# Kernel tuning notes

Hardware: AMD Instinct MI355X
Metric: run time of the kernel (lower is better)

## Reference

```python
import jax, jax.numpy as jnp
import numpy as np

N_M, N_E = 100_000, 50_000      # materials / elements node counts
FM, FE, H = 256, 64, 128        # raw feature dims, hidden_channels
E, EL = 1_000_000, 250_000      # message edges per direction, label edges per decoder


def setup_inputs() -> dict:
    key = jax.random.key(0)
    ks = jax.random.split(key, 40)

    def w(i, shape):
        fan_in = shape[0]
        return jax.random.normal(ks[i], shape, jnp.float32) / np.sqrt(fan_in)

    inp = {
        "x_materials": jax.random.normal(ks[0], (N_M, FM), jnp.float32),
        "x_elements": jax.random.normal(ks[1], (N_E, FE), jnp.float32),
        # message-passing edges: materials->elements and elements->materials
        "src_m2e": jax.random.randint(ks[2], (E,), 0, N_M),
        "dst_m2e": jax.random.randint(ks[3], (E,), 0, N_E),
        "src_e2m": jax.random.randint(ks[4], (E,), 0, N_E),
        "dst_e2m": jax.random.randint(ks[5], (E,), 0, N_M),
        # supervision (edge_label_index) per decoder
        "lbl_src_m2e": jax.random.randint(ks[6], (EL,), 0, N_M),
        "lbl_dst_m2e": jax.random.randint(ks[7], (EL,), 0, N_E),
        "lbl_src_e2m": jax.random.randint(ks[8], (EL,), 0, N_E),
        "lbl_dst_e2m": jax.random.randint(ks[9], (EL,), 0, N_M),
        # input projections per node type
        "Wp_m": w(10, (FM, H)), "bp_m": jnp.zeros((H,), jnp.float32),
        "Wp_e": w(11, (FE, H)), "bp_e": jnp.zeros((H,), jnp.float32),
        # SAGEConv per edge type: lin_l (neighbor, with bias) + lin_r (root, no bias)
        "Wl_m2e": w(12, (H, H)), "bl_m2e": jnp.zeros((H,), jnp.float32), "Wr_m2e": w(13, (H, H)),
        "Wl_e2m": w(14, (H, H)), "bl_e2m": jnp.zeros((H,), jnp.float32), "Wr_e2m": w(15, (H, H)),
        # ffw linear per node type (to_hetero duplicates per node type)
        "Wffw_m": w(16, (H, H)), "bffw_m": jnp.zeros((H,), jnp.float32),
        "Wffw_e": w(17, (H, H)), "bffw_e": jnp.zeros((H,), jnp.float32),
        # output proj per node type
        "Wproj_m": w(18, (H, H)), "bproj_m": jnp.zeros((H,), jnp.float32),
        "Wproj_e": w(19, (H, H)), "bproj_e": jnp.zeros((H,), jnp.float32),
        # edge decoders (concat -> 2H -> 2H relu -> 1 -> sigmoid), one per edge type
        "Wmlp_m2e": w(20, (2 * H, 2 * H)), "bmlp_m2e": jnp.zeros((2 * H,), jnp.float32),
        "Wout_m2e": w(21, (2 * H, 1)), "bout_m2e": jnp.zeros((1,), jnp.float32),
        "Wmlp_e2m": w(22, (2 * H, 2 * H)), "bmlp_e2m": jnp.zeros((2 * H,), jnp.float32),
        "Wout_e2m": w(23, (2 * H, 1)), "bout_e2m": jnp.zeros((1,), jnp.float32),
    }
    return inp


def _sage(x_src, x_dst, src, dst, Wl, bl, Wr):
    """SAGEConv(aggr='mean'): W_l @ mean_{j in N(i)} x_j + b_l + W_r @ x_i."""
    n_dst = x_dst.shape[0]
    agg = jax.ops.segment_sum(x_src[src], dst, num_segments=n_dst)          # [n_dst, H]
    cnt = jax.ops.segment_sum(jnp.ones(src.shape, x_src.dtype), dst, num_segments=n_dst)
    mean = agg / jnp.maximum(cnt, 1.0)[:, None]
    return mean @ Wl + bl + x_dst @ Wr


def _decode(zs, zd, W1, b1, W2, b2):
    z = jnp.concatenate([zs, zd], axis=-1)                                  # [EL, 2H]
    z = jax.nn.relu(z @ W1 + b1)
    return jax.nn.sigmoid((z @ W2 + b2)[:, 0])                              # [EL]


def reference(x_materials, x_elements,
              src_m2e, dst_m2e, src_e2m, dst_e2m,
              lbl_src_m2e, lbl_dst_m2e, lbl_src_e2m, lbl_dst_e2m,
              Wp_m, bp_m, Wp_e, bp_e,
              Wl_m2e, bl_m2e, Wr_m2e, Wl_e2m, bl_e2m, Wr_e2m,
              Wffw_m, bffw_m, Wffw_e, bffw_e,
              Wproj_m, bproj_m, Wproj_e, bproj_e,
              Wmlp_m2e, bmlp_m2e, Wout_m2e, bout_m2e,
              Wmlp_e2m, bmlp_e2m, Wout_e2m, bout_e2m):
    # process_input_nodes: per-type projections
    z_m = x_materials @ Wp_m + bp_m
    z_e = x_elements @ Wp_e + bp_e
    # hetero SAGEConv layer (each node type has exactly one incoming edge type)
    h_m = jax.nn.relu(_sage(z_e, z_m, src_e2m, dst_e2m, Wl_e2m, bl_e2m, Wr_e2m))
    h_e = jax.nn.relu(_sage(z_m, z_e, src_m2e, dst_m2e, Wl_m2e, bl_m2e, Wr_m2e))
    # ffw layer per node type
    h_m = jax.nn.relu(h_m @ Wffw_m + bffw_m)
    h_e = jax.nn.relu(h_e @ Wffw_e + bffw_e)
    # output projection per node type
    h_m = h_m @ Wproj_m + bproj_m
    h_e = h_e @ Wproj_e + bproj_e
    # per-edge-type decoders on supervision edges
    out_m2e = _decode(h_m[lbl_src_m2e], h_e[lbl_dst_m2e], Wmlp_m2e, bmlp_m2e, Wout_m2e, bout_m2e)
    out_e2m = _decode(h_e[lbl_src_e2m], h_m[lbl_dst_e2m], Wmlp_e2m, bmlp_e2m, Wout_e2m, bout_e2m)
    return out_m2e, out_e2m
```

## Files before the change

kernel.cpp:

```cpp
#include <hip/hip_runtime.h>
#include <math.h>

#define N_M 100000
#define N_E 50000
#define FM 256
#define FE 64
#define H 128
#define NEDGE 1000000
#define NLBL 250000

#define BUCK 128
#define NB_M ((N_M + BUCK - 1) / BUCK)
#define NB_E ((N_E + BUCK - 1) / BUCK)
#define CAP_M 2048
#define CAP_E 4096
#define CHUNK 8192

typedef unsigned short u16;
typedef unsigned int u32;
typedef short bf16x8 __attribute__((ext_vector_type(8)));
typedef float f32x4  __attribute__((ext_vector_type(4)));
typedef u16 u16x8    __attribute__((ext_vector_type(8)));
typedef u16 u16x4    __attribute__((ext_vector_type(4)));

__device__ __forceinline__ u16 f2bf(float x) {
    unsigned u = __float_as_uint(x);
    u += 0x7FFF + ((u >> 16) & 1);
    return (u16)(u >> 16);
}
__device__ __forceinline__ float bf2f(u16 h) {
    return __uint_as_float(((unsigned)h) << 16);
}

#define NPACK 14
struct PackDesc { const float* src; u16* dst; int K, N; };
struct PackArgs { PackDesc d[NPACK]; };

__global__ __launch_bounds__(64)
void pack_kernel(PackArgs args)
{
    PackDesc pd = args.d[blockIdx.y];
    int KT = pd.K / 32, NT = pd.N / 16;
    int tile = blockIdx.x;
    if (tile >= KT * NT) return;
    int kt = tile / NT, nt = tile % NT;
    int l = threadIdx.x;
    u16* dst = pd.dst + ((size_t)tile * 64 + l) * 8;
    #pragma unroll
    for (int j = 0; j < 8; ++j) {
        float v = pd.src[(size_t)(kt * 32 + (l >> 4) * 8 + j) * pd.N + nt * 16 + (l & 15)];
        dst[j] = f2bf(v);
    }
}

template<int K, int N, bool HAS_A2, bool RELU, bool A_FP32, bool HAS_BIAS>
__global__ __launch_bounds__(256)
void mfma_gemm(const void* __restrict__ A1, const void* __restrict__ A2,
               const u16* __restrict__ W1p, const u16* __restrict__ W2p,
               const float* __restrict__ bias, u16* __restrict__ C, int M)
{
    constexpr int NT = N / 16, KT = K / 32;
    const int wid = threadIdx.x >> 6, lane = threadIdx.x & 63;
    const int row0 = blockIdx.x * 64 + wid * 16;
    if (row0 >= M) return;
    const int l15 = lane & 15, l4 = lane >> 4;

    f32x4 acc[NT];
    #pragma unroll
    for (int nt = 0; nt < NT; ++nt) acc[nt] = (f32x4){0.f, 0.f, 0.f, 0.f};

    const int npass = HAS_A2 ? 2 : 1;
    for (int pass = 0; pass < npass; ++pass) {
        const void* A = pass ? A2 : A1;
        const u16* Wp = pass ? W2p : W1p;
        #pragma unroll
        for (int kt = 0; kt < KT; ++kt) {
            bf16x8 a;
            if constexpr (A_FP32) {
                const float* ap = (const float*)A + (size_t)(row0 + l15) * K + kt * 32 + l4 * 8;
                float4 f0 = *(const float4*)ap;
                float4 f1 = *(const float4*)(ap + 4);
                a[0] = (short)f2bf(f0.x); a[1] = (short)f2bf(f0.y);
                a[2] = (short)f2bf(f0.z); a[3] = (short)f2bf(f0.w);
                a[4] = (short)f2bf(f1.x); a[5] = (short)f2bf(f1.y);
                a[6] = (short)f2bf(f1.z); a[7] = (short)f2bf(f1.w);
            } else {
                a = *(const bf16x8*)((const u16*)A + (size_t)(row0 + l15) * K + kt * 32 + l4 * 8);
            }
            #pragma unroll
            for (int nt = 0; nt < NT; ++nt) {
                bf16x8 b = *(const bf16x8*)(Wp + ((size_t)(kt * NT + nt) * 64 + lane) * 8);
                acc[nt] = __builtin_amdgcn_mfma_f32_16x16x32_bf16(a, b, acc[nt], 0, 0, 0);
            }
        }
    }

    #pragma unroll
    for (int nt = 0; nt < NT; ++nt) {
        #pragma unroll
        for (int r = 0; r < 4; ++r) {
            int row = row0 + l4 * 4 + r;
            int col = nt * 16 + l15;
            float v = acc[nt][r];
            if (HAS_BIAS) v += bias[col];
            if (RELU) v = fmaxf(v, 0.f);
            C[(size_t)row * N + col] = f2bf(v);
        }
    }
}

__global__ __launch_bounds__(1024)
void bucket2_kernel(const int* __restrict__ src_a, const int* __restrict__ dst_a,
                    const int* __restrict__ src_b, const int* __restrict__ dst_b,
                    u32* __restrict__ pairs_a, int* __restrict__ gcur_a,
                    u32* __restrict__ pairs_b, int* __restrict__ gcur_b)
{
    __shared__ int cnt[1024];
    __shared__ int gbase[1024];

    const int dir = blockIdx.y;
    const int* __restrict__ src = dir ? src_b : src_a;
    const int* __restrict__ dst = dir ? dst_b : dst_a;
    u32* __restrict__ pairs = dir ? pairs_b : pairs_a;
    int* __restrict__ gcur  = dir ? gcur_b : gcur_a;
    const int NB  = dir ? NB_E : NB_M;
    const int CAP = dir ? CAP_E : CAP_M;

    const int tid = threadIdx.x;
    const int e0 = blockIdx.x * CHUNK;
    const int e1 = min(e0 + CHUNK, NEDGE);

    cnt[tid] = 0;
    __syncthreads();

    int myd[CHUNK / 1024];
    int k = 0;
    for (int e = e0 + tid; e < e1; e += 1024, ++k) {
        int d = dst[e];
        myd[k] = d;
        atomicAdd(&cnt[d >> 7], 1);
    }
    __syncthreads();

    if (tid < NB) {
        int c = cnt[tid];
        gbase[tid] = (c > 0) ? atomicAdd(&gcur[tid], c) : 0;
        cnt[tid] = 0;
    }
    __syncthreads();

    k = 0;
    for (int e = e0 + tid; e < e1; e += 1024, ++k) {
        int d = myd[k];
        int b = d >> 7;
        int p = gbase[b] + atomicAdd(&cnt[b], 1);
        if (p < CAP)
            pairs[(size_t)b * CAP + p] = ((u32)(d & (BUCK - 1)) << 24) | (u32)src[e];
    }
}

__global__ __launch_bounds__(256)
void bucket_mean2_kernel(const u16* __restrict__ z_a, const u32* __restrict__ pairs_a,
                         const int* __restrict__ gcur_a, u16* __restrict__ out_a,
                         const u16* __restrict__ z_b, const u32* __restrict__ pairs_b,
                         const int* __restrict__ gcur_b, u16* __restrict__ out_b)
{
    __shared__ int loc_src[CAP_E];
    __shared__ int cnt[BUCK], seg[BUCK], cur[BUCK];

    const int dir = blockIdx.y;
    const int b = blockIdx.x;
    if (dir && b >= NB_E) return;

    const u16* __restrict__ z     = dir ? z_b : z_a;
    const u32* __restrict__ pairs = dir ? pairs_b : pairs_a;
    const int* __restrict__ gcur  = dir ? gcur_b : gcur_a;
    u16* __restrict__ outm        = dir ? out_b : out_a;
    const int cap     = dir ? CAP_E : CAP_M;
    const int n_nodes = dir ? N_E : N_M;

    const int tid = threadIdx.x;
    const int n = min(gcur[b], cap);
    const u32* __restrict__ pb = pairs + (size_t)b * cap;

    if (tid < BUCK) cnt[tid] = 0;
    __syncthreads();
    for (int e = tid; e < n; e += 256)
        atomicAdd(&cnt[pb[e] >> 24], 1);
    __syncthreads();

    int myc = (tid < BUCK) ? cnt[tid] : 0;
    if (tid < BUCK) seg[tid] = myc;
    __syncthreads();
    for (int off = 1; off < BUCK; off <<= 1) {
        int t = 0;
        if (tid < BUCK && tid >= off) t = seg[tid - off];
        __syncthreads();
        if (tid < BUCK && tid >= off) seg[tid] += t;
        __syncthreads();
    }
    if (tid < BUCK) { int ex = seg[tid] - myc; seg[tid] = ex; cur[tid] = ex; }
    __syncthreads();

    for (int e = tid; e < n; e += 256) {
        u32 pk = pb[e];
        int p = atomicAdd(&cur[pk >> 24], 1);
        loc_src[p] = (int)(pk & 0xFFFFFF);
    }
    __syncthreads();

    const int grp = tid >> 5, lane = tid & 31;
    for (int loc = grp; loc < BUCK; loc += 8) {
        int gnode = b * BUCK + loc;
        if (gnode >= n_nodes) continue;
        int s0 = seg[loc], c = cnt[loc];
        float4 accA = {0.f, 0.f, 0.f, 0.f};
        float4 accB = {0.f, 0.f, 0.f, 0.f};
        int i = 0;
        for (; i + 2 <= c; i += 2) {
            int sA = loc_src[s0 + i];
            int sB = loc_src[s0 + i + 1];
            u16x4 vA = *(const u16x4*)&z[(size_t)sA * H + lane * 4];
            u16x4 vB = *(const u16x4*)&z[(size_t)sB * H + lane * 4];
            accA.x += bf2f(vA[0]); accA.y += bf2f(vA[1]);
            accA.z += bf2f(vA[2]); accA.w += bf2f(vA[3]);
            accB.x += bf2f(vB[0]); accB.y += bf2f(vB[1]);
            accB.z += bf2f(vB[2]); accB.w += bf2f(vB[3]);
        }
        if (i < c) {
            int sA = loc_src[s0 + i];
            u16x4 vA = *(const u16x4*)&z[(size_t)sA * H + lane * 4];
            accA.x += bf2f(vA[0]); accA.y += bf2f(vA[1]);
            accA.z += bf2f(vA[2]); accA.w += bf2f(vA[3]);
        }
        accA.x += accB.x; accA.y += accB.y; accA.z += accB.z; accA.w += accB.w;
        float inv = 1.0f / fmaxf((float)c, 1.0f);
        u16x4 o;
        o[0] = f2bf(accA.x * inv); o[1] = f2bf(accA.y * inv);
        o[2] = f2bf(accA.z * inv); o[3] = f2bf(accA.w * inv);
        *(u16x4*)&outm[(size_t)gnode * H + lane * 4] = o;
    }
}

#define EPQ 8
#define NQ  31250

__global__ __launch_bounds__(256)
void edge_decode_kernel(const u16* __restrict__ Us, const u16* __restrict__ Ud,
                        const int* __restrict__ lsrc, const int* __restrict__ ldst,
                        const float* __restrict__ b1, const float* __restrict__ W2,
                        const float* __restrict__ b2, float* __restrict__ out)
{
    const int t  = blockIdx.x * 256 + threadIdx.x;
    const int q  = t >> 4;
    const int li = t & 15;
    if (q >= NQ) return;

    float w2v[16], b1v[16];
    #pragma unroll
    for (int j = 0; j < 4; ++j) {
        float4 w = *(const float4*)&W2[li * 16 + j * 4];
        float4 bb = *(const float4*)&b1[li * 16 + j * 4];
        w2v[j*4+0] = w.x; w2v[j*4+1] = w.y; w2v[j*4+2] = w.z; w2v[j*4+3] = w.w;
        b1v[j*4+0] = bb.x; b1v[j*4+1] = bb.y; b1v[j*4+2] = bb.z; b1v[j*4+3] = bb.w;
    }
    const float bout = b2[0];

    #pragma unroll
    for (int i = 0; i < EPQ; ++i) {
        int e = q + i * NQ;
        int s = lsrc[e], d = ldst[e];
        const u16* us = Us + (size_t)s * 256 + li * 16;
        const u16* ud = Ud + (size_t)d * 256 + li * 16;
        u16x8 sa = *(const u16x8*)us;
        u16x8 sb = *(const u16x8*)(us + 8);
        u16x8 da = *(const u16x8*)ud;
        u16x8 db = *(const u16x8*)(ud + 8);
        float acc = 0.f;
        #pragma unroll
        for (int j = 0; j < 8; ++j)
            acc += fmaxf(bf2f(sa[j]) + bf2f(da[j]) + b1v[j], 0.f) * w2v[j];
        #pragma unroll
        for (int j = 0; j < 8; ++j)
            acc += fmaxf(bf2f(sb[j]) + bf2f(db[j]) + b1v[8 + j], 0.f) * w2v[8 + j];
        acc += __shfl_xor(acc, 1, 16);
        acc += __shfl_xor(acc, 2, 16);
        acc += __shfl_xor(acc, 4, 16);
        acc += __shfl_xor(acc, 8, 16);
        if (li == 0) out[e] = 1.0f / (1.0f + expf(-(acc + bout)));
    }
}

extern "C" void kernel_launch(void* const* d_in, const int* in_sizes, int n_in,
                              void* d_out, int out_size, void* d_ws, size_t ws_size,
                              hipStream_t stream)
{
    const float* x_m      = (const float*)d_in[0];
    const float* x_e      = (const float*)d_in[1];
    const int*   src_m2e  = (const int*)d_in[2];
    const int*   dst_m2e  = (const int*)d_in[3];
    const int*   src_e2m  = (const int*)d_in[4];
    const int*   dst_e2m  = (const int*)d_in[5];
    const int*   lsrc_m2e = (const int*)d_in[6];
    const int*   ldst_m2e = (const int*)d_in[7];
    const int*   lsrc_e2m = (const int*)d_in[8];
    const int*   ldst_e2m = (const int*)d_in[9];
    const float* Wp_m   = (const float*)d_in[10];
    const float* bp_m   = (const float*)d_in[11];
    const float* Wp_e   = (const float*)d_in[12];
    const float* bp_e   = (const float*)d_in[13];
    const float* Wl_m2e = (const float*)d_in[14];
    const float* bl_m2e = (const float*)d_in[15];
    const float* Wr_m2e = (const float*)d_in[16];
    const float* Wl_e2m = (const float*)d_in[17];
    const float* bl_e2m = (const float*)d_in[18];
    const float* Wr_e2m = (const float*)d_in[19];
    const float* Wffw_m = (const float*)d_in[20];
    const float* bffw_m = (const float*)d_in[21];
    const float* Wffw_e = (const float*)d_in[22];
    const float* bffw_e = (const float*)d_in[23];
    const float* Wproj_m = (const float*)d_in[24];
    const float* bproj_m = (const float*)d_in[25];
    const float* Wproj_e = (const float*)d_in[26];
    const float* bproj_e = (const float*)d_in[27];
    const float* Wmlp_m2e = (const float*)d_in[28];
    const float* bmlp_m2e = (const float*)d_in[29];
    const float* Wout_m2e = (const float*)d_in[30];
    const float* bout_m2e = (const float*)d_in[31];
    const float* Wmlp_e2m = (const float*)d_in[32];
    const float* bmlp_e2m = (const float*)d_in[33];
    const float* Wout_e2m = (const float*)d_in[34];
    const float* bout_e2m = (const float*)d_in[35];

    float* out = (float*)d_out;

    u16* B_m = (u16*)d_ws;
    u16* B_e = B_m + (size_t)N_M * H;
    u16* U0  = B_e + (size_t)N_E * H;
    u16* A_m = U0;
    u16* A_e = A_m + (size_t)N_M * H;
    u16* Us  = U0;
    u16* Ud  = U0 + (size_t)N_M * 256;
    u32* pairs_m = (u32*)(A_e + (size_t)N_E * H);
    u32* pairs_e = pairs_m + (size_t)NB_M * CAP_M;
    int* gcur_m  = (int*)(pairs_e + (size_t)NB_E * CAP_E);
    int* gcur_e  = gcur_m + NB_M;
    u16* pk = U0 + 2 * (size_t)N_M * 256;
    u16* pWp_m   = pk;  pk += 256 * 128;
    u16* pWp_e   = pk;  pk += 64 * 128;
    u16* pWl_e2m = pk;  pk += 128 * 128;
    u16* pWr_e2m = pk;  pk += 128 * 128;
    u16* pWl_m2e = pk;  pk += 128 * 128;
    u16* pWr_m2e = pk;  pk += 128 * 128;
    u16* pWffw_m = pk;  pk += 128 * 128;
    u16* pWffw_e = pk;  pk += 128 * 128;
    u16* pWproj_m= pk;  pk += 128 * 128;
    u16* pWproj_e= pk;  pk += 128 * 128;
    u16* pW1a_m2e= pk;  pk += 128 * 256;
    u16* pW1b_m2e= pk;  pk += 128 * 256;
    u16* pW1a_e2m= pk;  pk += 128 * 256;
    u16* pW1b_e2m= pk;  pk += 128 * 256;

    dim3 blk(256);
    dim3 gm((N_M + 63) / 64), ge((N_E + 63) / 64);

    PackArgs pa;
    pa.d[0]  = { Wp_m,               pWp_m,    FM, H };
    pa.d[1]  = { Wp_e,               pWp_e,    FE, H };
    pa.d[2]  = { Wl_e2m,             pWl_e2m,  H,  H };
    pa.d[3]  = { Wr_e2m,             pWr_e2m,  H,  H };
    pa.d[4]  = { Wl_m2e,             pWl_m2e,  H,  H };
    pa.d[5]  = { Wr_m2e,             pWr_m2e,  H,  H };
    pa.d[6]  = { Wffw_m,             pWffw_m,  H,  H };
    pa.d[7]  = { Wffw_e,             pWffw_e,  H,  H };
    pa.d[8]  = { Wproj_m,            pWproj_m, H,  H };
    pa.d[9]  = { Wproj_e,            pWproj_e, H,  H };
    pa.d[10] = { Wmlp_m2e,           pW1a_m2e, H,  256 };
    pa.d[11] = { Wmlp_m2e + 128*256, pW1b_m2e, H,  256 };
    pa.d[12] = { Wmlp_e2m,           pW1a_e2m, H,  256 };
    pa.d[13] = { Wmlp_e2m + 128*256, pW1b_e2m, H,  256 };
    pack_kernel<<<dim3(64, NPACK), dim3(64), 0, stream>>>(pa);

    mfma_gemm<FM, H, false, false, true, true><<<gm, blk, 0, stream>>>(
        x_m, nullptr, pWp_m, nullptr, bp_m, A_m, N_M);
    mfma_gemm<FE, H, false, false, true, true><<<ge, blk, 0, stream>>>(
        x_e, nullptr, pWp_e, nullptr, bp_e, A_e, N_E);

    hipMemsetAsync(gcur_m, 0, sizeof(int) * (NB_M + NB_E), stream);
    const int nbk = (NEDGE + CHUNK - 1) / CHUNK;
    bucket2_kernel<<<dim3(nbk, 2), dim3(1024), 0, stream>>>(
        src_e2m, dst_e2m, src_m2e, dst_m2e,
        pairs_m, gcur_m, pairs_e, gcur_e);

    bucket_mean2_kernel<<<dim3(NB_M, 2), blk, 0, stream>>>(
        A_e, pairs_m, gcur_m, B_m,
        A_m, pairs_e, gcur_e, B_e);

    mfma_gemm<H, H, true, true, false, true><<<gm, blk, 0, stream>>>(
        B_m, A_m, pWl_e2m, pWr_e2m, bl_e2m, B_m, N_M);
    mfma_gemm<H, H, true, true, false, true><<<ge, blk, 0, stream>>>(
        B_e, A_e, pWl_m2e, pWr_m2e, bl_m2e, B_e, N_E);

    mfma_gemm<H, H, false, true, false, true><<<gm, blk, 0, stream>>>(
        B_m, nullptr, pWffw_m, nullptr, bffw_m, A_m, N_M);
    mfma_gemm<H, H, false, true, false, true><<<ge, blk, 0, stream>>>(
        B_e, nullptr, pWffw_e, nullptr, bffw_e, A_e, N_E);

    mfma_gemm<H, H, false, false, false, true><<<gm, blk, 0, stream>>>(
        A_m, nullptr, pWproj_m, nullptr, bproj_m, B_m, N_M);
    mfma_gemm<H, H, false, false, false, true><<<ge, blk, 0, stream>>>(
        A_e, nullptr, pWproj_e, nullptr, bproj_e, B_e, N_E);

    dim3 gdq((NQ * 16 + 255) / 256);
    mfma_gemm<H, 256, false, false, false, false><<<gm, blk, 0, stream>>>(
        B_m, nullptr, pW1a_m2e, nullptr, nullptr, Us, N_M);
    mfma_gemm<H, 256, false, false, false, false><<<ge, blk, 0, stream>>>(
        B_e, nullptr, pW1b_m2e, nullptr, nullptr, Ud, N_E);
    edge_decode_kernel<<<gdq, blk, 0, stream>>>(
        Us, Ud, lsrc_m2e, ldst_m2e, bmlp_m2e, Wout_m2e, bout_m2e, out);

    mfma_gemm<H, 256, false, false, false, false><<<ge, blk, 0, stream>>>(
        B_e, nullptr, pW1a_e2m, nullptr, nullptr, Us, N_E);
    mfma_gemm<H, 256, false, false, false, false><<<gm, blk, 0, stream>>>(
        B_m, nullptr, pW1b_e2m, nullptr, nullptr, Ud, N_M);
    edge_decode_kernel<<<gdq, blk, 0, stream>>>(
        Us, Ud, lsrc_e2m, ldst_e2m, bmlp_e2m, Wout_e2m, bout_e2m, out + NLBL);
}
```

Measured before the change: 418.9 us.

## Fuse SAGE, FFW and projection GEMMs into one per-node-type chain kernel

Replaces the three back-to-back per-node-type GEMM launches (SAGE lin_l+lin_r with relu, ffw with relu, output proj) with one kernel that keeps each warp's 16-row intermediate in shared memory between stages. This removes two global round-trips of the 128-wide bf16 activations and four kernel launches. It also adds row clamping and bounds checks for partial tiles and simplifies the generic GEMM template by dropping the two-input and relu options. The cost is extra LDS use per block and serial dependent MFMA stages inside each warp.

```diff
diff --git a/kernel.cpp b/kernel.cpp
--- a/kernel.cpp
+++ b/kernel.cpp
@@ -53,10 +53,10 @@
     }
 }
 
-template<int K, int N, bool HAS_A2, bool RELU, bool A_FP32, bool HAS_BIAS>
+template<int K, int N, bool A_FP32, bool HAS_BIAS>
 __global__ __launch_bounds__(256)
-void mfma_gemm(const void* __restrict__ A1, const void* __restrict__ A2,
-               const u16* __restrict__ W1p, const u16* __restrict__ W2p,
+void mfma_gemm(const void* __restrict__ A1,
+               const u16* __restrict__ W1p,
                const float* __restrict__ bias, u16* __restrict__ C, int M)
 {
     constexpr int NT = N / 16, KT = K / 32;
@@ -69,29 +69,25 @@
     #pragma unroll
     for (int nt = 0; nt < NT; ++nt) acc[nt] = (f32x4){0.f, 0.f, 0.f, 0.f};
 
-    const int npass = HAS_A2 ? 2 : 1;
-    for (int pass = 0; pass < npass; ++pass) {
-        const void* A = pass ? A2 : A1;
-        const u16* Wp = pass ? W2p : W1p;
-        #pragma unroll
-        for (int kt = 0; kt < KT; ++kt) {
-            bf16x8 a;
-            if constexpr (A_FP32) {
-                const float* ap = (const float*)A + (size_t)(row0 + l15) * K + kt * 32 + l4 * 8;
-                float4 f0 = *(const float4*)ap;
-                float4 f1 = *(const float4*)(ap + 4);
-                a[0] = (short)f2bf(f0.x); a[1] = (short)f2bf(f0.y);
-                a[2] = (short)f2bf(f0.z); a[3] = (short)f2bf(f0.w);
-                a[4] = (short)f2bf(f1.x); a[5] = (short)f2bf(f1.y);
-                a[6] = (short)f2bf(f1.z); a[7] = (short)f2bf(f1.w);
-            } else {
-                a = *(const bf16x8*)((const u16*)A + (size_t)(row0 + l15) * K + kt * 32 + l4 * 8);
-            }
-            #pragma unroll
-            for (int nt = 0; nt < NT; ++nt) {
-                bf16x8 b = *(const bf16x8*)(Wp + ((size_t)(kt * NT + nt) * 64 + lane) * 8);
-                acc[nt] = __builtin_amdgcn_mfma_f32_16x16x32_bf16(a, b, acc[nt], 0, 0, 0);
-            }
+    const int ar = min(row0 + l15, M - 1);
+    #pragma unroll
+    for (int kt = 0; kt < KT; ++kt) {
+        bf16x8 a;
+        if constexpr (A_FP32) {
+            const float* ap = (const float*)A1 + (size_t)ar * K + kt * 32 + l4 * 8;
+            float4 f0 = *(const float4*)ap;
+            float4 f1 = *(const float4*)(ap + 4);
+            a[0] = (short)f2bf(f0.x); a[1] = (short)f2bf(f0.y);
+            a[2] = (short)f2bf(f0.z); a[3] = (short)f2bf(f0.w);
+            a[4] = (short)f2bf(f1.x); a[5] = (short)f2bf(f1.y);
+            a[6] = (short)f2bf(f1.z); a[7] = (short)f2bf(f1.w);
+        } else {
+            a = *(const bf16x8*)((const u16*)A1 + (size_t)ar * K + kt * 32 + l4 * 8);
+        }
+        #pragma unroll
+        for (int nt = 0; nt < NT; ++nt) {
+            bf16x8 b = *(const bf16x8*)(W1p + ((size_t)(kt * NT + nt) * 64 + lane) * 8);
+            acc[nt] = __builtin_amdgcn_mfma_f32_16x16x32_bf16(a, b, acc[nt], 0, 0, 0);
         }
     }
 
@@ -103,8 +99,93 @@
             int col = nt * 16 + l15;
             float v = acc[nt][r];
             if (HAS_BIAS) v += bias[col];
-            if (RELU) v = fmaxf(v, 0.f);
-            C[(size_t)row * N + col] = f2bf(v);
+            if (row < M) C[(size_t)row * N + col] = f2bf(v);
+        }
+    }
+}
+
+__global__ __launch_bounds__(256)
+void fused_chain_kernel(const u16* __restrict__ Bm, const u16* __restrict__ Az,
+                        const u16* __restrict__ pWl, const u16* __restrict__ pWr,
+                        const u16* __restrict__ pWffw, const u16* __restrict__ pWproj,
+                        const float* __restrict__ bl, const float* __restrict__ bffw,
+                        const float* __restrict__ bproj,
+                        u16* __restrict__ Bout, int M)
+{
+    constexpr int LDW = 136;
+    __shared__ __align__(16) u16 xp[4][16][LDW];
+
+    const int wid = threadIdx.x >> 6, lane = threadIdx.x & 63;
+    const int row0 = blockIdx.x * 64 + wid * 16;
+    if (row0 >= M) return;
+    const int l15 = lane & 15, l4 = lane >> 4;
+    const int ar = min(row0 + l15, M - 1);
+    u16 (* __restrict__ xw)[LDW] = xp[wid];
+
+    f32x4 acc[8];
+
+    #pragma unroll
+    for (int nt = 0; nt < 8; ++nt) acc[nt] = (f32x4){0.f, 0.f, 0.f, 0.f};
+    #pragma unroll
+    for (int kt = 0; kt < 4; ++kt) {
+        bf16x8 a1 = *(const bf16x8*)&Bm[(size_t)ar * H + kt * 32 + l4 * 8];
+        bf16x8 a2 = *(const bf16x8*)&Az[(size_t)ar * H + kt * 32 + l4 * 8];
+        #pragma unroll
+        for (int nt = 0; nt < 8; ++nt) {
+            bf16x8 b1 = *(const bf16x8*)&pWl[((size_t)(kt * 8 + nt) * 64 + lane) * 8];
+            bf16x8 b2 = *(const bf16x8*)&pWr[((size_t)(kt * 8 + nt) * 64 + lane) * 8];
+            acc[nt] = __builtin_amdgcn_mfma_f32_16x16x32_bf16(a1, b1, acc[nt], 0, 0, 0);
+            acc[nt] = __builtin_amdgcn_mfma_f32_16x16x32_bf16(a2, b2, acc[nt], 0, 0, 0);
+        }
+    }
+    #pragma unroll
+    for (int nt = 0; nt < 8; ++nt) {
+        int col = nt * 16 + l15;
+        float bv = bl[col];
+        #pragma unroll
+        for (int r = 0; r < 4; ++r)
+            xw[l4 * 4 + r][col] = f2bf(fmaxf(acc[nt][r] + bv, 0.f));
+    }
+
+    #pragma unroll
+    for (int nt = 0; nt < 8; ++nt) acc[nt] = (f32x4){0.f, 0.f, 0.f, 0.f};
+    #pragma unroll
+    for (int kt = 0; kt < 4; ++kt) {
+        bf16x8 a = *(const bf16x8*)&xw[l15][kt * 32 + l4 * 8];
+        #pragma unroll
+        for (int nt = 0; nt < 8; ++nt) {
+            bf16x8 b = *(const bf16x8*)&pWffw[((size_t)(kt * 8 + nt) * 64 + lane) * 8];
+            acc[nt] = __builtin_amdgcn_mfma_f32_16x16x32_bf16(a, b, acc[nt], 0, 0, 0);
+        }
+    }
+    #pragma unroll
+    for (int nt = 0; nt < 8; ++nt) {
+        int col = nt * 16 + l15;
+        float bv = bffw[col];
+        #pragma unroll
+        for (int r = 0; r < 4; ++r)
+            xw[l4 * 4 + r][col] = f2bf(fmaxf(acc[nt][r] + bv, 0.f));
+    }
+
+    #pragma unroll
+    for (int nt = 0; nt < 8; ++nt) acc[nt] = (f32x4){0.f, 0.f, 0.f, 0.f};
+    #pragma unroll
+    for (int kt = 0; kt < 4; ++kt) {
+        bf16x8 a = *(const bf16x8*)&xw[l15][kt * 32 + l4 * 8];
+        #pragma unroll
+        for (int nt = 0; nt < 8; ++nt) {
+            bf16x8 b = *(const bf16x8*)&pWproj[((size_t)(kt * 8 + nt) * 64 + lane) * 8];
+            acc[nt] = __builtin_amdgcn_mfma_f32_16x16x32_bf16(a, b, acc[nt], 0, 0, 0);
+        }
+    }
+    #pragma unroll
+    for (int nt = 0; nt < 8; ++nt) {
+        int col = nt * 16 + l15;
+        float bv = bproj[col];
+        #pragma unroll
+        for (int r = 0; r < 4; ++r) {
+            int row = row0 + l4 * 4 + r;
+            if (row < M) Bout[(size_t)row * H + col] = f2bf(acc[nt][r] + bv);
         }
     }
 }
@@ -381,10 +462,8 @@
     pa.d[13] = { Wmlp_e2m + 128*256, pW1b_e2m, H,  256 };
     pack_kernel<<<dim3(64, NPACK), dim3(64), 0, stream>>>(pa);
 
-    mfma_gemm<FM, H, false, false, true, true><<<gm, blk, 0, stream>>>(
-        x_m, nullptr, pWp_m, nullptr, bp_m, A_m, N_M);
-    mfma_gemm<FE, H, false, false, true, true><<<ge, blk, 0, stream>>>(
-        x_e, nullptr, pWp_e, nullptr, bp_e, A_e, N_E);
+    mfma_gemm<FM, H, true, true><<<gm, blk, 0, stream>>>(x_m, pWp_m, bp_m, A_m, N_M);
+    mfma_gemm<FE, H, true, true><<<ge, blk, 0, stream>>>(x_e, pWp_e, bp_e, A_e, N_E);
 
     hipMemsetAsync(gcur_m, 0, sizeof(int) * (NB_M + NB_E), stream);
     const int nbk = (NEDGE + CHUNK - 1) / CHUNK;
@@ -396,33 +475,21 @@
         A_e, pairs_m, gcur_m, B_m,
         A_m, pairs_e, gcur_e, B_e);
 
-    mfma_gemm<H, H, true, true, false, true><<<gm, blk, 0, stream>>>(
-        B_m, A_m, pWl_e2m, pWr_e2m, bl_e2m, B_m, N_M);
-    mfma_gemm<H, H, true, true, false, true><<<ge, blk, 0, stream>>>(
-        B_e, A_e, pWl_m2e, pWr_m2e, bl_m2e, B_e, N_E);
-
-    mfma_gemm<H, H, false, true, false, true><<<gm, blk, 0, stream>>>(
-        B_m, nullptr, pWffw_m, nullptr, bffw_m, A_m, N_M);
-    mfma_gemm<H, H, false, true, false, true><<<ge, blk, 0, stream>>>(
-        B_e, nullptr, pWffw_e, nullptr, bffw_e, A_e, N_E);
-
-    mfma_gemm<H, H, false, false, false, true><<<gm, blk, 0, stream>>>(
-        A_m, nullptr, pWproj_m, nullptr, bproj_m, B_m, N_M);
-    mfma_gemm<H, H, false, false, false, true><<<ge, blk, 0, stream>>>(
-        A_e, nullptr, pWproj_e, nullptr, bproj_e, B_e, N_E);
+    fused_chain_kernel<<<gm, blk, 0, stream>>>(
+        B_m, A_m, pWl_e2m, pWr_e2m, pWffw_m, pWproj_m,
+        bl_e2m, bffw_m, bproj_m, B_m, N_M);
+    fused_chain_kernel<<<ge, blk, 0, stream>>>(
+        B_e, A_e, pWl_m2e, pWr_m2e, pWffw_e, pWproj_e,
+        bl_m2e, bffw_e, bproj_e, B_e, N_E);
 
     dim3 gdq((NQ * 16 + 255) / 256);
-    mfma_gemm<H, 256, false, false, false, false><<<gm, blk, 0, stream>>>(
-        B_m, nullptr, pW1a_m2e, nullptr, nullptr, Us, N_M);
-    mfma_gemm<H, 256, false, false, false, false><<<ge, blk, 0, stream>>>(
-        B_e, nullptr, pW1b_m2e, nullptr, nullptr, Ud, N_E);
+    mfma_gemm<H, 256, false, false><<<gm, blk, 0, stream>>>(B_m, pW1a_m2e, nullptr, Us, N_M);
+    mfma_gemm<H, 256, false, false><<<ge, blk, 0, stream>>>(B_e, pW1b_m2e, nullptr, Ud, N_E);
     edge_decode_kernel<<<gdq, blk, 0, stream>>>(
         Us, Ud, lsrc_m2e, ldst_m2e, bmlp_m2e, Wout_m2e, bout_m2e, out);
 
-    mfma_gemm<H, 256, false, false, false, false><<<ge, blk, 0, stream>>>(
-        B_e, nullptr, pW1a_e2m, nullptr, nullptr, Us, N_E);
-    mfma_gemm<H, 256, false, false, false, false><<<gm, blk, 0, stream>>>(
-        B_m, nullptr, pW1b_e2m, nullptr, nullptr, Ud, N_M);
+    mfma_gemm<H, 256, false, false><<<ge, blk, 0, stream>>>(B_e, pW1a_e2m, nullptr, Us, N_E);
+    mfma_gemm<H, 256, false, false><<<gm, blk, 0, stream>>>(B_m, pW1b_e2m, nullptr, Ud, N_M);
     edge_decode_kernel<<<gdq, blk, 0, stream>>>(
         Us, Ud, lsrc_e2m, ldst_e2m, bmlp_e2m, Wout_e2m, bout_e2m, out + NLBL);
 }
```

Measured after the change: 447.8 us. 6.9% more time.

## Fuse decoder first layer into per-edge MFMA decode kernel

Applied to the files above, without the earlier changes.

Replaces the per-node precompute of the decoder's first layer (four GEMMs writing 256-wide intermediates) with a single edge kernel. It gathers the source and destination embeddings per label edge and runs the 256x256 layer with bf16 MFMA in-kernel, then applies ReLU, the output dot and the sigmoid. This removes the large intermediate writes and halves the per-edge gather width. In exchange it recomputes the layer per edge, roughly tripling the FLOPs, and uses many accumulator registers.

```diff
diff --git a/kernel.cpp b/kernel.cpp
--- a/kernel.cpp
+++ b/kernel.cpp
@@ -32,7 +32,7 @@
     return __uint_as_float(((unsigned)h) << 16);
 }
 
-#define NPACK 14
+#define NPACK 12
 struct PackDesc { const float* src; u16* dst; int K, N; };
 struct PackArgs { PackDesc d[NPACK]; };
 
@@ -242,52 +242,75 @@
     }
 }
 
-#define EPQ 8
-#define NQ  31250
-
 __global__ __launch_bounds__(256)
-void edge_decode_kernel(const u16* __restrict__ Us, const u16* __restrict__ Ud,
-                        const int* __restrict__ lsrc, const int* __restrict__ ldst,
-                        const float* __restrict__ b1, const float* __restrict__ W2,
-                        const float* __restrict__ b2, float* __restrict__ out)
-{
-    const int t  = blockIdx.x * 256 + threadIdx.x;
-    const int q  = t >> 4;
-    const int li = t & 15;
-    if (q >= NQ) return;
-
-    float w2v[16], b1v[16];
-    #pragma unroll
-    for (int j = 0; j < 4; ++j) {
-        float4 w = *(const float4*)&W2[li * 16 + j * 4];
-        float4 bb = *(const float4*)&b1[li * 16 + j * 4];
-        w2v[j*4+0] = w.x; w2v[j*4+1] = w.y; w2v[j*4+2] = w.z; w2v[j*4+3] = w.w;
-        b1v[j*4+0] = bb.x; b1v[j*4+1] = bb.y; b1v[j*4+2] = bb.z; b1v[j*4+3] = bb.w;
+void edge_decode_mfma_kernel(const u16* __restrict__ hs, const u16* __restrict__ hd,
+                             const int* __restrict__ lsrc, const int* __restrict__ ldst,
+                             const u16* __restrict__ W1p,
+                             const float* __restrict__ b1, const float* __restrict__ W2,
+                             const float* __restrict__ b2, float* __restrict__ out)
+{
+    const int wid = threadIdx.x >> 6, lane = threadIdx.x & 63;
+    const int l15 = lane & 15, l4 = lane >> 4;
+    const int e0 = (blockIdx.x * 4 + wid) * 32;
+    if (e0 >= NLBL) return;
+
+    float b1v[16], w2v[16];
+    #pragma unroll
+    for (int nt = 0; nt < 16; ++nt) {
+        b1v[nt] = b1[nt * 16 + l15];
+        w2v[nt] = W2[nt * 16 + l15];
     }
     const float bout = b2[0];
 
-    #pragma unroll
-    for (int i = 0; i < EPQ; ++i) {
-        int e = q + i * NQ;
-        int s = lsrc[e], d = ldst[e];
-        const u16* us = Us + (size_t)s * 256 + li * 16;
-        const u16* ud = Ud + (size_t)d * 256 + li * 16;
-        u16x8 sa = *(const u16x8*)us;
-        u16x8 sb = *(const u16x8*)(us + 8);
-        u16x8 da = *(const u16x8*)ud;
-        u16x8 db = *(const u16x8*)(ud + 8);
-        float acc = 0.f;
+    const int eA = min(e0 + l15, NLBL - 1);
+    const int eB = min(e0 + 16 + l15, NLBL - 1);
+    const int sA = lsrc[eA], dA = ldst[eA];
+    const int sB = lsrc[eB], dB = ldst[eB];
+
+    f32x4 acc0[16], acc1[16];
+    #pragma unroll
+    for (int nt = 0; nt < 16; ++nt) {
+        acc0[nt] = (f32x4){0.f, 0.f, 0.f, 0.f};
+        acc1[nt] = (f32x4){0.f, 0.f, 0.f, 0.f};
+    }
+
+    #pragma unroll
+    for (int kt = 0; kt < 8; ++kt) {
+        const int off = kt * 32 + l4 * 8;
+        bf16x8 a0, a1;
+        if (off < H) {
+            a0 = *(const bf16x8*)&hs[(size_t)sA * H + off];
+            a1 = *(const bf16x8*)&hs[(size_t)sB * H + off];
+        } else {
+            a0 = *(const bf16x8*)&hd[(size_t)dA * H + off - H];
+            a1 = *(const bf16x8*)&hd[(size_t)dB * H + off - H];
+        }
         #pragma unroll
-        for (int j = 0; j < 8; ++j)
-            acc += fmaxf(bf2f(sa[j]) + bf2f(da[j]) + b1v[j], 0.f) * w2v[j];
+        for (int nt = 0; nt < 16; ++nt) {
+            bf16x8 b = *(const bf16x8*)&W1p[((size_t)(kt * 16 + nt) * 64 + lane) * 8];
+            acc0[nt] = __builtin_amdgcn_mfma_f32_16x16x32_bf16(a0, b, acc0[nt], 0, 0, 0);
+            acc1[nt] = __builtin_amdgcn_mfma_f32_16x16x32_bf16(a1, b, acc1[nt], 0, 0, 0);
+        }
+    }
+
+    #pragma unroll
+    for (int r = 0; r < 4; ++r) {
+        float p0 = 0.f, p1 = 0.f;
         #pragma unroll
-        for (int j = 0; j < 8; ++j)
-            acc += fmaxf(bf2f(sb[j]) + bf2f(db[j]) + b1v[8 + j], 0.f) * w2v[8 + j];
-        acc += __shfl_xor(acc, 1, 16);
-        acc += __shfl_xor(acc, 2, 16);
-        acc += __shfl_xor(acc, 4, 16);
-        acc += __shfl_xor(acc, 8, 16);
-        if (li == 0) out[e] = 1.0f / (1.0f + expf(-(acc + bout)));
+        for (int nt = 0; nt < 16; ++nt) {
+            p0 += fmaxf(acc0[nt][r] + b1v[nt], 0.f) * w2v[nt];
+            p1 += fmaxf(acc1[nt][r] + b1v[nt], 0.f) * w2v[nt];
+        }
+        p0 += __shfl_xor(p0, 1, 16); p0 += __shfl_xor(p0, 2, 16);
+        p0 += __shfl_xor(p0, 4, 16); p0 += __shfl_xor(p0, 8, 16);
+        p1 += __shfl_xor(p1, 1, 16); p1 += __shfl_xor(p1, 2, 16);
+        p1 += __shfl_xor(p1, 4, 16); p1 += __shfl_xor(p1, 8, 16);
+        if (l15 == 0) {
+            int ea = e0 + l4 * 4 + r;
+            int eb = ea + 16;
+            if (ea < NLBL) out[ea] = 1.0f / (1.0f + expf(-(p0 + bout)));
+            if (eb < NLBL) out[eb] = 1.0f / (1.0f + expf(-(p1 + bout)));
+        }
     }
 }
 
@@ -336,16 +359,13 @@
 
     u16* B_m = (u16*)d_ws;
     u16* B_e = B_m + (size_t)N_M * H;
-    u16* U0  = B_e + (size_t)N_E * H;
-    u16* A_m = U0;
+    u16* A_m = B_e + (size_t)N_E * H;
     u16* A_e = A_m + (size_t)N_M * H;
-    u16* Us  = U0;
-    u16* Ud  = U0 + (size_t)N_M * 256;
     u32* pairs_m = (u32*)(A_e + (size_t)N_E * H);
     u32* pairs_e = pairs_m + (size_t)NB_M * CAP_M;
     int* gcur_m  = (int*)(pairs_e + (size_t)NB_E * CAP_E);
     int* gcur_e  = gcur_m + NB_M;
-    u16* pk = U0 + 2 * (size_t)N_M * 256;
+    u16* pk = (u16*)(gcur_e + NB_E);
     u16* pWp_m   = pk;  pk += 256 * 128;
     u16* pWp_e   = pk;  pk += 64 * 128;
     u16* pWl_e2m = pk;  pk += 128 * 128;
@@ -356,30 +376,26 @@
     u16* pWffw_e = pk;  pk += 128 * 128;
     u16* pWproj_m= pk;  pk += 128 * 128;
     u16* pWproj_e= pk;  pk += 128 * 128;
-    u16* pW1a_m2e= pk;  pk += 128 * 256;
-    u16* pW1b_m2e= pk;  pk += 128 * 256;
-    u16* pW1a_e2m= pk;  pk += 128 * 256;
-    u16* pW1b_e2m= pk;  pk += 128 * 256;
+    u16* pW1_m2e = pk;  pk += 256 * 256;
+    u16* pW1_e2m = pk;  pk += 256 * 256;
 
     dim3 blk(256);
     dim3 gm((N_M + 63) / 64), ge((N_E + 63) / 64);
 
     PackArgs pa;
-    pa.d[0]  = { Wp_m,               pWp_m,    FM, H };
-    pa.d[1]  = { Wp_e,               pWp_e,    FE, H };
-    pa.d[2]  = { Wl_e2m,             pWl_e2m,  H,  H };
-    pa.d[3]  = { Wr_e2m,             pWr_e2m,  H,  H };
-    pa.d[4]  = { Wl_m2e,             pWl_m2e,  H,  H };
-    pa.d[5]  = { Wr_m2e,             pWr_m2e,  H,  H };
-    pa.d[6]  = { Wffw_m,             pWffw_m,  H,  H };
-    pa.d[7]  = { Wffw_e,             pWffw_e,  H,  H };
-    pa.d[8]  = { Wproj_m,            pWproj_m, H,  H };
-    pa.d[9]  = { Wproj_e,            pWproj_e, H,  H };
-    pa.d[10] = { Wmlp_m2e,           pW1a_m2e, H,  256 };
-    pa.d[11] = { Wmlp_m2e + 128*256, pW1b_m2e, H,  256 };
-    pa.d[12] = { Wmlp_e2m,           pW1a_e2m, H,  256 };
-    pa.d[13] = { Wmlp_e2m + 128*256, pW1b_e2m, H,  256 };
-    pack_kernel<<<dim3(64, NPACK), dim3(64), 0, stream>>>(pa);
+    pa.d[0]  = { Wp_m,     pWp_m,    FM,  H };
+    pa.d[1]  = { Wp_e,     pWp_e,    FE,  H };
+    pa.d[2]  = { Wl_e2m,   pWl_e2m,  H,   H };
+    pa.d[3]  = { Wr_e2m,   pWr_e2m,  H,   H };
+    pa.d[4]  = { Wl_m2e,   pWl_m2e,  H,   H };
+    pa.d[5]  = { Wr_m2e,   pWr_m2e,  H,   H };
+    pa.d[6]  = { Wffw_m,   pWffw_m,  H,   H };
+    pa.d[7]  = { Wffw_e,   pWffw_e,  H,   H };
+    pa.d[8]  = { Wproj_m,  pWproj_m, H,   H };
+    pa.d[9]  = { Wproj_e,  pWproj_e, H,   H };
+    pa.d[10] = { Wmlp_m2e, pW1_m2e,  256, 256 };
+    pa.d[11] = { Wmlp_e2m, pW1_e2m,  256, 256 };
+    pack_kernel<<<dim3(128, NPACK), dim3(64), 0, stream>>>(pa);
 
     mfma_gemm<FM, H, false, false, true, true><<<gm, blk, 0, stream>>>(
         x_m, nullptr, pWp_m, nullptr, bp_m, A_m, N_M);
@@ -411,18 +427,9 @@
     mfma_gemm<H, H, false, false, false, true><<<ge, blk, 0, stream>>>(
         A_e, nullptr, pWproj_e, nullptr, bproj_e, B_e, N_E);
 
-    dim3 gdq((NQ * 16 + 255) / 256);
-    mfma_gemm<H, 256, false, false, false, false><<<gm, blk, 0, stream>>>(
-        B_m, nullptr, pW1a_m2e, nullptr, nullptr, Us, N_M);
-    mfma_gemm<H, 256, false, false, false, false><<<ge, blk, 0, stream>>>(
-        B_e, nullptr, pW1b_m2e, nullptr, nullptr, Ud, N_E);
-    edge_decode_kernel<<<gdq, blk, 0, stream>>>(
-        Us, Ud, lsrc_m2e, ldst_m2e, bmlp_m2e, Wout_m2e, bout_m2e, out);
-
-    mfma_gemm<H, 256, false, false, false, false><<<ge, blk, 0, stream>>>(
-        B_e, nullptr, pW1a_e2m, nullptr, nullptr, Us, N_E);
-    mfma_gemm<H, 256, false, false, false, false><<<gm, blk, 0, stream>>>(
-        B_m, nullptr, pW1b_e2m, nullptr, nullptr, Ud, N_M);
-    edge_decode_kernel<<<gdq, blk, 0, stream>>>(
-        Us, Ud, lsrc_e2m, ldst_e2m, bmlp_e2m, Wout_e2m, bout_e2m, out + NLBL);
-}
+    dim3 gdec((NLBL + 127) / 128);
+    edge_decode_mfma_kernel<<<gdec, blk, 0, stream>>>(
+        B_m, B_e, lsrc_m2e, ldst_m2e, pW1_m2e, bmlp_m2e, Wout_m2e, bout_m2e, out);
+    edge_decode_mfma_kernel<<<gdec, blk, 0, stream>>>(
+        B_e, B_m, lsrc_e2m, ldst_e2m, pW1_e2m, bmlp_e2m, Wout_e2m, bout_e2m, out + NLBL);
+}
```

After: 448.3 us. 7.0% more time.
